# Optimization experiments

Hardware: AMD Instinct MI355X
Metric: run time of the kernel (lower is better)

Reference implementation:

```python
import jax, jax.numpy as jnp
import numpy as np

B, S, D = 4, 8192, 1024
NC = 5
EPS = 1e-5  # nn.LayerNorm default eps


def setup_inputs() -> dict:
    key = jax.random.key(0)
    kx, kid, kg, kb, ks, kw, kbias = jax.random.split(key, 7)
    x = jax.random.normal(kx, (B, S, D), dtype=jnp.float32)
    compartment_ids = jax.random.randint(kid, (B, S), 0, NC)
    # per-compartment LayerNorm affine params (stacked) and scaling
    gamma = 1.0 + 0.1 * jax.random.normal(kg, (NC, D), dtype=jnp.float32)
    beta = 0.1 * jax.random.normal(kb, (NC, D), dtype=jnp.float32)
    scale = 1.0 + 0.1 * jax.random.normal(ks, (NC,), dtype=jnp.float32)
    # compartment_transition_norm: nn.Linear(d_model, d_model)
    W = jax.random.normal(kw, (D, D), dtype=jnp.float32) / np.sqrt(D)
    b = 0.01 * jax.random.normal(kbias, (D,), dtype=jnp.float32)
    return {"x": x, "compartment_ids": compartment_ids, "gamma": gamma,
            "beta": beta, "scale": scale, "W": W, "b": b}


def reference(x, compartment_ids, gamma, beta, scale, W, b):
    # tokens with id >= NC are left untouched (original guard)
    valid = compartment_ids < NC                      # [B,S]
    cid = jnp.clip(compartment_ids, 0, NC - 1)        # safe gather index
    # per-token LayerNorm statistics over last dim (biased variance)
    mu = jnp.mean(x, axis=-1, keepdims=True)
    var = jnp.mean(jnp.square(x - mu), axis=-1, keepdims=True)
    normed = (x - mu) * jax.lax.rsqrt(var + EPS)      # [B,S,D]
    g = gamma[cid]                                    # [B,S,D]
    bt = beta[cid]                                    # [B,S,D]
    s = scale[cid][..., None]                         # [B,S,1]
    y = (normed * g + bt) * s
    y = jnp.where(valid[..., None], y, x)
    # residual transition: x + Linear(x)
    return y + jnp.einsum('bsd,ed->bse', y, W) + b
```

## Files before the change

kernel.cpp:

```cpp
#include <hip/hip_runtime.h>
#include <stdint.h>

#define NCOMP 5
#define DM 1024
#define LN_EPS 1e-5f

typedef __attribute__((ext_vector_type(8))) __bf16 bf16x8;
typedef __attribute__((ext_vector_type(4))) float f32x4;

__device__ __forceinline__ unsigned short f2bf(float f) {
    unsigned u = __builtin_bit_cast(unsigned, f);
    u += 0x7fffu + ((u >> 16) & 1u);
    return (unsigned short)(u >> 16);
}
__device__ __forceinline__ float bf2f(unsigned short h) {
    return __builtin_bit_cast(float, ((unsigned)h) << 16);
}

__global__ __launch_bounds__(128) void ln_kernel(
    const float* __restrict__ x, const int* __restrict__ cid,
    const float* __restrict__ gamma, const float* __restrict__ beta,
    const float* __restrict__ scale, unsigned short* __restrict__ y)
{
    const int t = blockIdx.x;
    const int tid = threadIdx.x;
    const float* xp = x + (size_t)t * DM + tid * 8;
    const float4 a = *(const float4*)xp;
    const float4 b = *(const float4*)(xp + 4);
    float s  = a.x + a.y + a.z + a.w + b.x + b.y + b.z + b.w;
    float ss = a.x*a.x + a.y*a.y + a.z*a.z + a.w*a.w
             + b.x*b.x + b.y*b.y + b.z*b.z + b.w*b.w;
#pragma unroll
    for (int off = 32; off > 0; off >>= 1) {
        s  += __shfl_down(s, off);
        ss += __shfl_down(ss, off);
    }
    __shared__ float red[4];
    if ((tid & 63) == 0) { red[tid >> 6] = s; red[2 + (tid >> 6)] = ss; }
    __syncthreads();
    const float sum = red[0] + red[1];
    const float sqs = red[2] + red[3];
    const float mu  = sum * (1.0f / DM);
    const float var = sqs * (1.0f / DM) - mu * mu;
    const float rs  = rsqrtf(var + LN_EPS);
    const int craw  = cid[t];
    const bool valid = craw < NCOMP;
    const int c = min(max(craw, 0), NCOMP - 1);
    const float sc = scale[c];
    const float* gp = gamma + c * DM + tid * 8;
    const float* bp = beta  + c * DM + tid * 8;
    const float4 g0 = *(const float4*)gp;
    const float4 g1 = *(const float4*)(gp + 4);
    const float4 b0 = *(const float4*)bp;
    const float4 b1 = *(const float4*)(bp + 4);
    float o[8];
    o[0] = valid ? ((a.x - mu) * rs * g0.x + b0.x) * sc : a.x;
    o[1] = valid ? ((a.y - mu) * rs * g0.y + b0.y) * sc : a.y;
    o[2] = valid ? ((a.z - mu) * rs * g0.z + b0.z) * sc : a.z;
    o[3] = valid ? ((a.w - mu) * rs * g0.w + b0.w) * sc : a.w;
    o[4] = valid ? ((b.x - mu) * rs * g1.x + b1.x) * sc : b.x;
    o[5] = valid ? ((b.y - mu) * rs * g1.y + b1.y) * sc : b.y;
    o[6] = valid ? ((b.z - mu) * rs * g1.z + b1.z) * sc : b.z;
    o[7] = valid ? ((b.w - mu) * rs * g1.w + b1.w) * sc : b.w;
    uint4 p;
    p.x = (unsigned)f2bf(o[0]) | ((unsigned)f2bf(o[1]) << 16);
    p.y = (unsigned)f2bf(o[2]) | ((unsigned)f2bf(o[3]) << 16);
    p.z = (unsigned)f2bf(o[4]) | ((unsigned)f2bf(o[5]) << 16);
    p.w = (unsigned)f2bf(o[6]) | ((unsigned)f2bf(o[7]) << 16);
    *(uint4*)(y + (size_t)t * DM + tid * 8) = p;
}

__global__ __launch_bounds__(256) void cvt_kernel(
    const float* __restrict__ W, unsigned short* __restrict__ Wb)
{
    const int i = (blockIdx.x * 256 + threadIdx.x) * 4;
    const float4 v = *(const float4*)(W + i);
    uint2 p;
    p.x = (unsigned)f2bf(v.x) | ((unsigned)f2bf(v.y) << 16);
    p.y = (unsigned)f2bf(v.z) | ((unsigned)f2bf(v.w) << 16);
    *(uint2*)(Wb + i) = p;
}

__device__ __forceinline__ void gld_lds16(const unsigned short* g, unsigned short* l) {
    __builtin_amdgcn_global_load_lds(
        (const __attribute__((address_space(1))) unsigned int*)(uintptr_t)g,
        (__attribute__((address_space(3))) unsigned int*)(uintptr_t)l,
        16, 0, 0);
}

__global__ __launch_bounds__(256) void gemm_kernel(
    const unsigned short* __restrict__ A,
    const unsigned short* __restrict__ Bt,
    const float* __restrict__ bias,
    float* __restrict__ C, int M)
{
    constexpr int K = 1024, N = 1024, BK = 32, TM = 128, TN = 128;
    __shared__ __align__(16) unsigned short smem[TM * BK + TN * BK];
    unsigned short* As = smem;
    unsigned short* Bs = smem + TM * BK;

    const int tid  = threadIdx.x;
    const int bm   = blockIdx.x * TM;
    const int bn   = blockIdx.y * TN;
    const int lane = tid & 63;
    const int wave = tid >> 6;
    const int wm   = (wave >> 1) * 64;
    const int wn   = (wave & 1) * 64;

    const int r0 = tid >> 2;
    const int c0 = (tid & 3) * 8;
    const unsigned short* Ag  = A  + (size_t)(bm + r0) * K + c0;
    const unsigned short* Ag2 = A  + (size_t)(bm + 64 + r0) * K + c0;
    const unsigned short* Bg  = Bt + (size_t)(bn + r0) * K + c0;
    const unsigned short* Bg2 = Bt + (size_t)(bn + 64 + r0) * K + c0;
    unsigned short* Asl  = &As[(size_t)tid * 8];
    unsigned short* Asl2 = &As[(size_t)(tid + 256) * 8];
    unsigned short* Bsl  = &Bs[(size_t)tid * 8];
    unsigned short* Bsl2 = &Bs[(size_t)(tid + 256) * 8];

    f32x4 acc[4][4] = {};

    const int quad = lane >> 4;
    const int qk = quad * 8;
    const int fr = lane & 15;

    for (int k0 = 0; k0 < K; k0 += BK) {
        __syncthreads();
        gld_lds16(Ag  + k0, Asl);
        gld_lds16(Ag2 + k0, Asl2);
        gld_lds16(Bg  + k0, Bsl);
        gld_lds16(Bg2 + k0, Bsl2);
        __syncthreads();

        bf16x8 af[4], bfr[4];
#pragma unroll
        for (int i = 0; i < 4; i++)
            af[i] = *(const bf16x8*)&As[(wm + i * 16 + fr) * BK + qk];
#pragma unroll
        for (int i = 0; i < 4; i++)
            bfr[i] = *(const bf16x8*)&Bs[(wn + i * 16 + fr) * BK + qk];
#pragma unroll
        for (int mi = 0; mi < 4; mi++)
#pragma unroll
            for (int ni = 0; ni < 4; ni++)
                acc[mi][ni] = __builtin_amdgcn_mfma_f32_16x16x32_bf16(
                    af[mi], bfr[ni], acc[mi][ni], 0, 0, 0);
    }

    __syncthreads();
    float* tb = (float*)smem + wave * 1024;
    const int erow = lane >> 3;
    const int ecol = (lane & 7) * 4;
#pragma unroll
    for (int mi = 0; mi < 4; mi++) {
#pragma unroll
        for (int ni = 0; ni < 4; ni++)
#pragma unroll
            for (int r = 0; r < 4; r++)
                tb[(quad * 4 + r) * 64 + ni * 16 + fr] = acc[mi][ni][r];
        __syncthreads();
#pragma unroll
        for (int j = 0; j < 4; j++) {
            const int row = (j >> 1) * 8 + erow;
            const int col = (j & 1) * 32 + ecol;
            const int gr = bm + wm + mi * 16 + row;
            const int gc = bn + wn + col;
            const float4 v = *(const float4*)&tb[row * 64 + col];
            const ushort4 yv = *(const ushort4*)(A + (size_t)gr * K + gc);
            const float4 bv = *(const float4*)&bias[gc];
            float4 o;
            o.x = v.x + bf2f(yv.x) + bv.x;
            o.y = v.y + bf2f(yv.y) + bv.y;
            o.z = v.z + bf2f(yv.z) + bv.z;
            o.w = v.w + bf2f(yv.w) + bv.w;
            *(float4*)&C[(size_t)gr * N + gc] = o;
        }
        __syncthreads();
    }
}

extern "C" void kernel_launch(void* const* d_in, const int* in_sizes, int n_in,
                              void* d_out, int out_size, void* d_ws, size_t ws_size,
                              hipStream_t stream)
{
    const float* x     = (const float*)d_in[0];
    const int*   cid   = (const int*)d_in[1];
    const float* gamma = (const float*)d_in[2];
    const float* beta  = (const float*)d_in[3];
    const float* scale = (const float*)d_in[4];
    const float* W     = (const float*)d_in[5];
    const float* bias  = (const float*)d_in[6];
    float* out = (float*)d_out;

    const int M = in_sizes[0] / DM;
    unsigned short* yb = (unsigned short*)d_ws;
    unsigned short* Wb = yb + (size_t)M * DM;

    ln_kernel<<<M, 128, 0, stream>>>(x, cid, gamma, beta, scale, yb);
    cvt_kernel<<<(DM * DM) / 1024, 256, 0, stream>>>(W, Wb);
    dim3 grid(M / 128, DM / 128);
    gemm_kernel<<<grid, 256, 0, stream>>>(yb, Wb, bias, out, M);
}
```

Measured before the change: 360.2 us.

## Fold residual into W+I, fuse LN with W convert, double-buffer GEMM loads

The residual add is moved into the weights by adding the identity to W during bf16 conversion, so the GEMM epilogue no longer reloads the bf16 activations. The LayerNorm and weight-conversion kernels are merged into one launch that handles four rows per block. The GEMM main loop becomes double-buffered in LDS with one barrier per k-step, and the epilogue staging gets padding, hoisted bias loads and fewer barriers. The residual now passes through bf16 inside the matmul instead of being added after it, which changes rounding. The epilogue also drops the barrier after the per-wave staging writes and relies on each wave touching only its own region.

Result: faster. 344.8 us (-4.3%).

```diff
diff --git a/kernel.cpp b/kernel.cpp
--- a/kernel.cpp
+++ b/kernel.cpp
@@ -13,72 +13,78 @@
     u += 0x7fffu + ((u >> 16) & 1u);
     return (unsigned short)(u >> 16);
 }
-__device__ __forceinline__ float bf2f(unsigned short h) {
-    return __builtin_bit_cast(float, ((unsigned)h) << 16);
-}
-
-__global__ __launch_bounds__(128) void ln_kernel(
+
+__global__ __launch_bounds__(128) void ln_w_kernel(
     const float* __restrict__ x, const int* __restrict__ cid,
     const float* __restrict__ gamma, const float* __restrict__ beta,
-    const float* __restrict__ scale, unsigned short* __restrict__ y)
+    const float* __restrict__ scale, const float* __restrict__ W,
+    unsigned short* __restrict__ y, unsigned short* __restrict__ Wb, int M)
 {
-    const int t = blockIdx.x;
     const int tid = threadIdx.x;
-    const float* xp = x + (size_t)t * DM + tid * 8;
-    const float4 a = *(const float4*)xp;
-    const float4 b = *(const float4*)(xp + 4);
-    float s  = a.x + a.y + a.z + a.w + b.x + b.y + b.z + b.w;
-    float ss = a.x*a.x + a.y*a.y + a.z*a.z + a.w*a.w
-             + b.x*b.x + b.y*b.y + b.z*b.z + b.w*b.w;
-#pragma unroll
-    for (int off = 32; off > 0; off >>= 1) {
-        s  += __shfl_down(s, off);
-        ss += __shfl_down(ss, off);
-    }
-    __shared__ float red[4];
-    if ((tid & 63) == 0) { red[tid >> 6] = s; red[2 + (tid >> 6)] = ss; }
-    __syncthreads();
-    const float sum = red[0] + red[1];
-    const float sqs = red[2] + red[3];
-    const float mu  = sum * (1.0f / DM);
-    const float var = sqs * (1.0f / DM) - mu * mu;
-    const float rs  = rsqrtf(var + LN_EPS);
-    const int craw  = cid[t];
-    const bool valid = craw < NCOMP;
-    const int c = min(max(craw, 0), NCOMP - 1);
-    const float sc = scale[c];
-    const float* gp = gamma + c * DM + tid * 8;
-    const float* bp = beta  + c * DM + tid * 8;
-    const float4 g0 = *(const float4*)gp;
-    const float4 g1 = *(const float4*)(gp + 4);
-    const float4 b0 = *(const float4*)bp;
-    const float4 b1 = *(const float4*)(bp + 4);
-    float o[8];
-    o[0] = valid ? ((a.x - mu) * rs * g0.x + b0.x) * sc : a.x;
-    o[1] = valid ? ((a.y - mu) * rs * g0.y + b0.y) * sc : a.y;
-    o[2] = valid ? ((a.z - mu) * rs * g0.z + b0.z) * sc : a.z;
-    o[3] = valid ? ((a.w - mu) * rs * g0.w + b0.w) * sc : a.w;
-    o[4] = valid ? ((b.x - mu) * rs * g1.x + b1.x) * sc : b.x;
-    o[5] = valid ? ((b.y - mu) * rs * g1.y + b1.y) * sc : b.y;
-    o[6] = valid ? ((b.z - mu) * rs * g1.z + b1.z) * sc : b.z;
-    o[7] = valid ? ((b.w - mu) * rs * g1.w + b1.w) * sc : b.w;
-    uint4 p;
-    p.x = (unsigned)f2bf(o[0]) | ((unsigned)f2bf(o[1]) << 16);
-    p.y = (unsigned)f2bf(o[2]) | ((unsigned)f2bf(o[3]) << 16);
-    p.z = (unsigned)f2bf(o[4]) | ((unsigned)f2bf(o[5]) << 16);
-    p.w = (unsigned)f2bf(o[6]) | ((unsigned)f2bf(o[7]) << 16);
-    *(uint4*)(y + (size_t)t * DM + tid * 8) = p;
-}
-
-__global__ __launch_bounds__(256) void cvt_kernel(
-    const float* __restrict__ W, unsigned short* __restrict__ Wb)
-{
-    const int i = (blockIdx.x * 256 + threadIdx.x) * 4;
-    const float4 v = *(const float4*)(W + i);
-    uint2 p;
-    p.x = (unsigned)f2bf(v.x) | ((unsigned)f2bf(v.y) << 16);
-    p.y = (unsigned)f2bf(v.z) | ((unsigned)f2bf(v.w) << 16);
-    *(uint2*)(Wb + i) = p;
+    __shared__ float red[8];
+    const int base = blockIdx.x * 4;
+#pragma unroll
+    for (int u = 0; u < 4; u++) {
+        const int t = base + u;
+        if (t < M) {
+            const float* xp = x + (size_t)t * DM + tid * 8;
+            const float4 a = *(const float4*)xp;
+            const float4 b = *(const float4*)(xp + 4);
+            float s  = a.x + a.y + a.z + a.w + b.x + b.y + b.z + b.w;
+            float ss = a.x*a.x + a.y*a.y + a.z*a.z + a.w*a.w
+                     + b.x*b.x + b.y*b.y + b.z*b.z + b.w*b.w;
+#pragma unroll
+            for (int off = 32; off > 0; off >>= 1) {
+                s  += __shfl_down(s, off);
+                ss += __shfl_down(ss, off);
+            }
+            float* rr = red + (u & 1) * 4;
+            if ((tid & 63) == 0) { rr[tid >> 6] = s; rr[2 + (tid >> 6)] = ss; }
+            __syncthreads();
+            const float mu  = (rr[0] + rr[1]) * (1.0f / DM);
+            const float var = (rr[2] + rr[3]) * (1.0f / DM) - mu * mu;
+            const float rs  = rsqrtf(var + LN_EPS);
+            const int craw  = cid[t];
+            const bool valid = craw < NCOMP;
+            const int c = min(max(craw, 0), NCOMP - 1);
+            const float sc = scale[c];
+            const float* gp = gamma + c * DM + tid * 8;
+            const float* bp = beta  + c * DM + tid * 8;
+            const float4 g0 = *(const float4*)gp;
+            const float4 g1 = *(const float4*)(gp + 4);
+            const float4 b0 = *(const float4*)bp;
+            const float4 b1 = *(const float4*)(bp + 4);
+            float o[8];
+            o[0] = valid ? ((a.x - mu) * rs * g0.x + b0.x) * sc : a.x;
+            o[1] = valid ? ((a.y - mu) * rs * g0.y + b0.y) * sc : a.y;
+            o[2] = valid ? ((a.z - mu) * rs * g0.z + b0.z) * sc : a.z;
+            o[3] = valid ? ((a.w - mu) * rs * g0.w + b0.w) * sc : a.w;
+            o[4] = valid ? ((b.x - mu) * rs * g1.x + b1.x) * sc : b.x;
+            o[5] = valid ? ((b.y - mu) * rs * g1.y + b1.y) * sc : b.y;
+            o[6] = valid ? ((b.z - mu) * rs * g1.z + b1.z) * sc : b.z;
+            o[7] = valid ? ((b.w - mu) * rs * g1.w + b1.w) * sc : b.w;
+            uint4 p;
+            p.x = (unsigned)f2bf(o[0]) | ((unsigned)f2bf(o[1]) << 16);
+            p.y = (unsigned)f2bf(o[2]) | ((unsigned)f2bf(o[3]) << 16);
+            p.z = (unsigned)f2bf(o[4]) | ((unsigned)f2bf(o[5]) << 16);
+            p.w = (unsigned)f2bf(o[6]) | ((unsigned)f2bf(o[7]) << 16);
+            *(uint4*)(y + (size_t)t * DM + tid * 8) = p;
+        } else {
+            const int row = t - M;
+            const float* wp = W + (size_t)row * DM + tid * 8;
+            const float4 a = *(const float4*)wp;
+            const float4 b = *(const float4*)(wp + 4);
+            float o[8] = {a.x, a.y, a.z, a.w, b.x, b.y, b.z, b.w};
+            const int d = row - tid * 8;
+            if (d >= 0 && d < 8) o[d] += 1.0f;
+            uint4 p;
+            p.x = (unsigned)f2bf(o[0]) | ((unsigned)f2bf(o[1]) << 16);
+            p.y = (unsigned)f2bf(o[2]) | ((unsigned)f2bf(o[3]) << 16);
+            p.z = (unsigned)f2bf(o[4]) | ((unsigned)f2bf(o[5]) << 16);
+            p.w = (unsigned)f2bf(o[6]) | ((unsigned)f2bf(o[7]) << 16);
+            *(uint4*)(Wb + (size_t)row * DM + tid * 8) = p;
+        }
+    }
 }
 
 __device__ __forceinline__ void gld_lds16(const unsigned short* g, unsigned short* l) {
@@ -90,18 +96,16 @@
 
 __global__ __launch_bounds__(256) void gemm_kernel(
     const unsigned short* __restrict__ A,
-    const unsigned short* __restrict__ Bt,
+    const unsigned short* __restrict__ Bp,
     const float* __restrict__ bias,
     float* __restrict__ C, int M)
 {
-    constexpr int K = 1024, N = 1024, BK = 32, TM = 128, TN = 128;
-    __shared__ __align__(16) unsigned short smem[TM * BK + TN * BK];
-    unsigned short* As = smem;
-    unsigned short* Bs = smem + TM * BK;
+    constexpr int K = 1024, N = 1024, BK = 32, TM = 128, NIT = K / BK;
+    __shared__ __align__(16) unsigned short smem[16384];
 
     const int tid  = threadIdx.x;
     const int bm   = blockIdx.x * TM;
-    const int bn   = blockIdx.y * TN;
+    const int bn   = blockIdx.y * TM;
     const int lane = tid & 63;
     const int wave = tid >> 6;
     const int wm   = (wave >> 1) * 64;
@@ -111,71 +115,75 @@
     const int c0 = (tid & 3) * 8;
     const unsigned short* Ag  = A  + (size_t)(bm + r0) * K + c0;
     const unsigned short* Ag2 = A  + (size_t)(bm + 64 + r0) * K + c0;
-    const unsigned short* Bg  = Bt + (size_t)(bn + r0) * K + c0;
-    const unsigned short* Bg2 = Bt + (size_t)(bn + 64 + r0) * K + c0;
-    unsigned short* Asl  = &As[(size_t)tid * 8];
-    unsigned short* Asl2 = &As[(size_t)(tid + 256) * 8];
-    unsigned short* Bsl  = &Bs[(size_t)tid * 8];
-    unsigned short* Bsl2 = &Bs[(size_t)(tid + 256) * 8];
+    const unsigned short* Bg  = Bp + (size_t)(bn + r0) * K + c0;
+    const unsigned short* Bg2 = Bp + (size_t)(bn + 64 + r0) * K + c0;
 
     f32x4 acc[4][4] = {};
-
     const int quad = lane >> 4;
     const int qk = quad * 8;
     const int fr = lane & 15;
 
-    for (int k0 = 0; k0 < K; k0 += BK) {
-        __syncthreads();
-        gld_lds16(Ag  + k0, Asl);
-        gld_lds16(Ag2 + k0, Asl2);
-        gld_lds16(Bg  + k0, Bsl);
-        gld_lds16(Bg2 + k0, Bsl2);
-        __syncthreads();
-
+    {
+        unsigned short* s = smem;
+        gld_lds16(Ag, s + (size_t)tid * 8);
+        gld_lds16(Ag2, s + (size_t)(tid + 256) * 8);
+        gld_lds16(Bg, s + 4096 + (size_t)tid * 8);
+        gld_lds16(Bg2, s + 4096 + (size_t)(tid + 256) * 8);
+    }
+    __syncthreads();
+
+#pragma unroll 2
+    for (int i = 0; i < NIT; i++) {
+        if (i + 1 < NIT) {
+            const int kn = (i + 1) * BK;
+            unsigned short* s = smem + ((i + 1) & 1) * 8192;
+            gld_lds16(Ag  + kn, s + (size_t)tid * 8);
+            gld_lds16(Ag2 + kn, s + (size_t)(tid + 256) * 8);
+            gld_lds16(Bg  + kn, s + 4096 + (size_t)tid * 8);
+            gld_lds16(Bg2 + kn, s + 4096 + (size_t)(tid + 256) * 8);
+        }
+        const unsigned short* As = smem + (i & 1) * 8192;
+        const unsigned short* Bs = As + 4096;
         bf16x8 af[4], bfr[4];
 #pragma unroll
-        for (int i = 0; i < 4; i++)
-            af[i] = *(const bf16x8*)&As[(wm + i * 16 + fr) * BK + qk];
-#pragma unroll
-        for (int i = 0; i < 4; i++)
-            bfr[i] = *(const bf16x8*)&Bs[(wn + i * 16 + fr) * BK + qk];
+        for (int j = 0; j < 4; j++)
+            af[j] = *(const bf16x8*)&As[(wm + j * 16 + fr) * BK + qk];
+#pragma unroll
+        for (int j = 0; j < 4; j++)
+            bfr[j] = *(const bf16x8*)&Bs[(wn + j * 16 + fr) * BK + qk];
 #pragma unroll
         for (int mi = 0; mi < 4; mi++)
 #pragma unroll
             for (int ni = 0; ni < 4; ni++)
                 acc[mi][ni] = __builtin_amdgcn_mfma_f32_16x16x32_bf16(
                     af[mi], bfr[ni], acc[mi][ni], 0, 0, 0);
-    }
-
-    __syncthreads();
-    float* tb = (float*)smem + wave * 1024;
+        __syncthreads();
+    }
+
+    float* tb = (float*)smem + wave * 1088;
     const int erow = lane >> 3;
     const int ecol = (lane & 7) * 4;
+    float4 bv0 = *(const float4*)&bias[bn + wn + ecol];
+    float4 bv1 = *(const float4*)&bias[bn + wn + 32 + ecol];
 #pragma unroll
     for (int mi = 0; mi < 4; mi++) {
 #pragma unroll
         for (int ni = 0; ni < 4; ni++)
 #pragma unroll
             for (int r = 0; r < 4; r++)
-                tb[(quad * 4 + r) * 64 + ni * 16 + fr] = acc[mi][ni][r];
-        __syncthreads();
+                tb[(quad * 4 + r) * 68 + ni * 16 + fr] = acc[mi][ni][r];
 #pragma unroll
         for (int j = 0; j < 4; j++) {
-            const int row = (j >> 1) * 8 + erow;
-            const int col = (j & 1) * 32 + ecol;
+            const int row  = (j >> 1) * 8 + erow;
+            const int colg = (j & 1) * 32 + ecol;
             const int gr = bm + wm + mi * 16 + row;
-            const int gc = bn + wn + col;
-            const float4 v = *(const float4*)&tb[row * 64 + col];
-            const ushort4 yv = *(const ushort4*)(A + (size_t)gr * K + gc);
-            const float4 bv = *(const float4*)&bias[gc];
+            const float4 v = *(const float4*)&tb[row * 68 + colg];
+            const float4 bv = (j & 1) ? bv1 : bv0;
             float4 o;
-            o.x = v.x + bf2f(yv.x) + bv.x;
-            o.y = v.y + bf2f(yv.y) + bv.y;
-            o.z = v.z + bf2f(yv.z) + bv.z;
-            o.w = v.w + bf2f(yv.w) + bv.w;
-            *(float4*)&C[(size_t)gr * N + gc] = o;
+            o.x = v.x + bv.x; o.y = v.y + bv.y;
+            o.z = v.z + bv.z; o.w = v.w + bv.w;
+            *(float4*)&C[(size_t)gr * N + bn + wn + colg] = o;
         }
-        __syncthreads();
     }
 }
 
@@ -196,8 +204,7 @@
     unsigned short* yb = (unsigned short*)d_ws;
     unsigned short* Wb = yb + (size_t)M * DM;
 
-    ln_kernel<<<M, 128, 0, stream>>>(x, cid, gamma, beta, scale, yb);
-    cvt_kernel<<<(DM * DM) / 1024, 256, 0, stream>>>(W, Wb);
+    ln_w_kernel<<<(M + DM) / 4, 128, 0, stream>>>(x, cid, gamma, beta, scale, W, yb, Wb, M);
     dim3 grid(M / 128, DM / 128);
     gemm_kernel<<<grid, 256, 0, stream>>>(yb, Wb, bias, out, M);
 }
```
